# Optimization experiments

Hardware: AMD Instinct MI355X
Metric: run time of the kernel (lower is better)

## Reference

```python
import jax, jax.numpy as jnp
import numpy as np

BS, N1, N2, OUT = 1024, 512, 512, 1024

def setup_inputs() -> dict:
    key = jax.random.key(0)
    k1, k2, k3 = jax.random.split(key, 3)
    x = jax.random.normal(k1, (BS, N1), dtype=jnp.float32)
    y = jax.random.normal(k2, (BS, N2), dtype=jnp.float32)
    # torch nn.Linear weight: [out_features, in_features], in = N1*N2 + N1 + N2
    W = jax.random.normal(k3, (OUT, N1 * N2 + N1 + N2), dtype=jnp.float32) * (1.0 / np.sqrt(N1 * N2 + N1 + N2))
    return {"x": x, "y": y, "W": W}

def reference(x, y, W):
    bs = x.shape[0]
    # outer product per sample, flattened row-major like torch matmul(x1, x2).view(bs,-1)
    x12 = jnp.einsum('bi,bj->bij', x, y).reshape(bs, -1)  # [bs, N1*N2]
    feat = jnp.concatenate([x, y, x12], axis=-1)           # [bs, N1+N2+N1*N2]
    return feat @ W.T                                      # [bs, OUT]
```

## Files before the change

### kernel.cpp

```cpp
#include <hip/hip_runtime.h>
#include <hip/hip_bf16.h>

#define N1C   512
#define N2C   512
#define MC    1024
#define NOUTC 1024
#define WROWC 263168
#define QOFFC 1024
#define NPHASE 129
#define NSPLIT 16

typedef __attribute__((ext_vector_type(8))) short bf16x8;
typedef __attribute__((ext_vector_type(4))) float f32x4;

union FragU { bf16x8 v; __hip_bfloat162 h2[4]; };

__device__ __forceinline__ __hip_bfloat162 cvt2(float a, float b) {
    return __float22bfloat162_rn(make_float2(a, b));
}

__device__ __forceinline__ void stage_direct(short* dst, const float* src) {
    f32x4 a = *(const f32x4*)src;
    f32x4 b = *(const f32x4*)(src + 4);
    FragU f;
    f.h2[0] = cvt2(a[0], a[1]); f.h2[1] = cvt2(a[2], a[3]);
    f.h2[2] = cvt2(b[0], b[1]); f.h2[3] = cvt2(b[2], b[3]);
    *(bf16x8*)dst = f.v;
}

__global__ __launch_bounds__(256) void transpose_x(const float* __restrict__ x,
                                                   float* __restrict__ xT) {
    __shared__ float t[64][65];
    const int i0 = blockIdx.x * 64;
    const int m0 = blockIdx.y * 64;
    const int tx = threadIdx.x & 63;
    const int ty = threadIdx.x >> 6;
#pragma unroll
    for (int k = 0; k < 16; ++k)
        t[ty * 16 + k][tx] = x[(size_t)(m0 + ty * 16 + k) * N1C + i0 + tx];
    __syncthreads();
#pragma unroll
    for (int k = 0; k < 16; ++k)
        xT[(size_t)(i0 + ty * 16 + k) * MC + m0 + tx] = t[tx][ty * 16 + k];
}

__global__ __launch_bounds__(256) void reduce_parts(const float* __restrict__ part,
                                                    float* __restrict__ out) {
    const size_t idx = ((size_t)blockIdx.x * 256 + threadIdx.x) * 4;
    f32x4 s = *(const f32x4*)(part + idx);
#pragma unroll
    for (int j = 1; j < NSPLIT; ++j)
        s += *(const f32x4*)(part + (size_t)j * (MC * NOUTC) + idx);
    *(f32x4*)(out + idx) = s;
}

template<bool USE_XT, bool USE_WS>
__global__ __launch_bounds__(256, 2) void quad_gemm(
        const float* __restrict__ x, const float* __restrict__ y,
        const float* __restrict__ W, const float* __restrict__ xT,
        float* __restrict__ out)
{
    __shared__ short sB[2][4][64][40];
    __shared__ float sX[2][4][512];

    const int tid  = threadIdx.x;
    const int wave = tid >> 6;
    const int lane = tid & 63;
    const int quad = lane >> 4;
    const int l15  = lane & 15;

    const int bid   = blockIdx.x;
    const int xcd   = bid & 7;
    const int useq  = bid >> 3;
    const int mh    = useq & 1;
    const int slice = (useq >> 1) + (xcd << 5);
    const int n0 = (slice & 15) << 6;
    const int jw = slice >> 4;
    const int j0 = jw << 5;
    const int m0 = mh << 9;

    const int mbase  = m0 + wave * 128 + l15;
    const int lrbase = wave * 128 + l15;

    float yf[8][8];
#pragma unroll
    for (int s = 0; s < 8; ++s) {
        const float* yp = y + (size_t)(mbase + s * 16) * N2C + (j0 + quad * 8);
        f32x4 a = *(const f32x4*)yp;
        f32x4 b = *(const f32x4*)(yp + 4);
#pragma unroll
        for (int t = 0; t < 4; ++t) { yf[s][t] = a[t]; yf[s][4 + t] = b[t]; }
    }

    f32x4 acc[8][4];
#pragma unroll
    for (int s = 0; s < 8; ++s)
#pragma unroll
        for (int un = 0; un < 4; ++un)
            acc[s][un] = {0.0f, 0.0f, 0.0f, 0.0f};

    const int sr  = tid >> 2;
    const int sc8 = (tid & 3) * 8;
    const float* wrow = W + (size_t)(n0 + sr) * WROWC + sc8;

    const int iix   = tid >> 6;
    const int lanex = tid & 63;

    stage_direct(&sB[0][0][sr][sc8], wrow + j0);
    stage_direct(&sB[0][1][sr][sc8], wrow + N1C + j0);
    {
        const int kc0 = QOFFC + j0;
#pragma unroll
        for (int ii = 0; ii < 4; ++ii)
            stage_direct(&sB[1][ii][sr][sc8], wrow + kc0 + (ii << 9));
    }
    if constexpr (USE_XT) {
        const float* xs = xT + (size_t)iix * MC + m0 + lanex * 8;
        f32x4 a = *(const f32x4*)xs;
        f32x4 b = *(const f32x4*)(xs + 4);
        *(f32x4*)&sX[1][iix][lanex * 8]     = a;
        *(f32x4*)&sX[1][iix][lanex * 8 + 4] = b;
    }
    __syncthreads();

    {
        bf16x8 afr[8];
#pragma unroll
        for (int s = 0; s < 8; ++s) {
            const float* xp = x + (size_t)(mbase + s * 16) * N1C + (j0 + quad * 8);
            f32x4 a = *(const f32x4*)xp;
            f32x4 b = *(const f32x4*)(xp + 4);
            FragU f;
            f.h2[0] = cvt2(a[0], a[1]); f.h2[1] = cvt2(a[2], a[3]);
            f.h2[2] = cvt2(b[0], b[1]); f.h2[3] = cvt2(b[2], b[3]);
            afr[s] = f.v;
        }
        {
            bf16x8 bfr[4];
#pragma unroll
            for (int un = 0; un < 4; ++un)
                bfr[un] = *(const bf16x8*)&sB[0][0][un * 16 + l15][quad * 8];
#pragma unroll
            for (int s = 0; s < 8; ++s)
#pragma unroll
                for (int un = 0; un < 4; ++un)
                    acc[s][un] = __builtin_amdgcn_mfma_f32_16x16x32_bf16(afr[s], bfr[un], acc[s][un], 0, 0, 0);
        }
#pragma unroll
        for (int s = 0; s < 8; ++s) {
            FragU f;
            f.h2[0] = cvt2(yf[s][0], yf[s][1]); f.h2[1] = cvt2(yf[s][2], yf[s][3]);
            f.h2[2] = cvt2(yf[s][4], yf[s][5]); f.h2[3] = cvt2(yf[s][6], yf[s][7]);
            afr[s] = f.v;
        }
        {
            bf16x8 bfr[4];
#pragma unroll
            for (int un = 0; un < 4; ++un)
                bfr[un] = *(const bf16x8*)&sB[0][1][un * 16 + l15][quad * 8];
#pragma unroll
            for (int s = 0; s < 8; ++s)
#pragma unroll
                for (int un = 0; un < 4; ++un)
                    acc[s][un] = __builtin_amdgcn_mfma_f32_16x16x32_bf16(afr[s], bfr[un], acc[s][un], 0, 0, 0);
        }
    }

    for (int p = 1; p < NPHASE; ++p) {
        const int cur = p & 1;
        const int nxt = cur ^ 1;
        const bool pref = (p + 1 < NPHASE);

        f32x4 wra[4], wrb[4], xra, xrb;
        if (pref) {
            const int kc0 = QOFFC + (p << 11) + j0;
#pragma unroll
            for (int ii = 0; ii < 4; ++ii) {
                const float* src = wrow + kc0 + (ii << 9);
                wra[ii] = *(const f32x4*)src;
                wrb[ii] = *(const f32x4*)(src + 4);
            }
            if constexpr (USE_XT) {
                const float* xs = xT + (size_t)((p << 2) + iix) * MC + m0 + lanex * 8;
                xra = *(const f32x4*)xs;
                xrb = *(const f32x4*)(xs + 4);
            }
        }

        f32x4 xq[8];
        if constexpr (!USE_XT) {
            const int ibase = (p - 1) * 4;
#pragma unroll
            for (int s = 0; s < 8; ++s)
                xq[s] = *(const f32x4*)(x + (size_t)(mbase + s * 16) * N1C + ibase);
        }

#pragma unroll
        for (int ii = 0; ii < 4; ++ii) {
            bf16x8 bfr[4];
#pragma unroll
            for (int un = 0; un < 4; ++un)
                bfr[un] = *(const bf16x8*)&sB[cur][ii][un * 16 + l15][quad * 8];
#pragma unroll
            for (int s = 0; s < 8; ++s) {
                float xs_v;
                if constexpr (USE_XT) xs_v = sX[cur][ii][lrbase + s * 16];
                else                  xs_v = xq[s][ii];
                FragU f;
                f.h2[0] = cvt2(xs_v * yf[s][0], xs_v * yf[s][1]);
                f.h2[1] = cvt2(xs_v * yf[s][2], xs_v * yf[s][3]);
                f.h2[2] = cvt2(xs_v * yf[s][4], xs_v * yf[s][5]);
                f.h2[3] = cvt2(xs_v * yf[s][6], xs_v * yf[s][7]);
#pragma unroll
                for (int un = 0; un < 4; ++un)
                    acc[s][un] = __builtin_amdgcn_mfma_f32_16x16x32_bf16(f.v, bfr[un], acc[s][un], 0, 0, 0);
            }
        }

        if (pref) {
#pragma unroll
            for (int ii = 0; ii < 4; ++ii) {
                FragU f;
                f.h2[0] = cvt2(wra[ii][0], wra[ii][1]); f.h2[1] = cvt2(wra[ii][2], wra[ii][3]);
                f.h2[2] = cvt2(wrb[ii][0], wrb[ii][1]); f.h2[3] = cvt2(wrb[ii][2], wrb[ii][3]);
                *(bf16x8*)&sB[nxt][ii][sr][sc8] = f.v;
            }
            if constexpr (USE_XT) {
                *(f32x4*)&sX[nxt][iix][lanex * 8]     = xra;
                *(f32x4*)&sX[nxt][iix][lanex * 8 + 4] = xrb;
            }
        }
        __syncthreads();
    }

    if constexpr (USE_WS) {
        float* dst = out + (size_t)jw * (MC * NOUTC);
#pragma unroll
        for (int s = 0; s < 8; ++s) {
            const int row0 = m0 + wave * 128 + s * 16 + quad * 4;
#pragma unroll
            for (int un = 0; un < 4; ++un) {
                const int col = n0 + un * 16 + l15;
#pragma unroll
                for (int r = 0; r < 4; ++r)
                    dst[(size_t)(row0 + r) * NOUTC + col] = acc[s][un][r];
            }
        }
    } else {
#pragma unroll
        for (int s = 0; s < 8; ++s) {
            const int row0 = m0 + wave * 128 + s * 16 + quad * 4;
#pragma unroll
            for (int un = 0; un < 4; ++un) {
                const int col = n0 + un * 16 + l15;
#pragma unroll
                for (int r = 0; r < 4; ++r)
                    atomicAdd(out + (size_t)(row0 + r) * NOUTC + col, acc[s][un][r]);
            }
        }
    }
}

extern "C" void kernel_launch(void* const* d_in, const int* in_sizes, int n_in,
                              void* d_out, int out_size, void* d_ws, size_t ws_size,
                              hipStream_t stream) {
    const float* x = (const float*)d_in[0];
    const float* y = (const float*)d_in[1];
    const float* W = (const float*)d_in[2];
    float* out = (float*)d_out;

    const size_t XT_BYTES   = (size_t)N1C * MC * sizeof(float);
    const size_t PART_BYTES = (size_t)NSPLIT * MC * NOUTC * sizeof(float);
    const bool haveXT = ws_size >= XT_BYTES;
    const bool haveWS = ws_size >= XT_BYTES + PART_BYTES;

    float* xT   = (float*)d_ws;
    float* part = (float*)((char*)d_ws + XT_BYTES);

    if (haveXT)
        transpose_x<<<dim3(N1C / 64, MC / 64), dim3(256), 0, stream>>>(x, xT);

    if (haveWS) {
        quad_gemm<true, true><<<dim3(512), dim3(256), 0, stream>>>(x, y, W, xT, part);
        reduce_parts<<<dim3((MC * NOUTC) / (256 * 4)), dim3(256), 0, stream>>>(part, out);
    } else {
        (void)hipMemsetAsync(out, 0, (size_t)out_size * sizeof(float), stream);
        if (haveXT)
            quad_gemm<true, false><<<dim3(512), dim3(256), 0, stream>>>(x, y, W, xT, out);
        else
            quad_gemm<false, false><<<dim3(512), dim3(256), 0, stream>>>(x, y, W, nullptr, out);
    }
}
```

Before: 2.266 ms.

## Split work across 8 waves with smaller per-wave tiles and quarter-M blocks

Each block now covers a quarter of M (256 rows) instead of half, and uses 512 threads arranged as a 4x2 wave grid. Each wave computes a 64x32 tile, so accumulator and y-fragment registers shrink and more waves can be resident per CU. The block count doubles, so the weight slices are staged twice as often overall. The shared-memory x-transpose buffer is dropped: x values are now read straight from the transposed global copy in each phase, which adds global or cache traffic in the inner loop but removes LDS stores and reads.

```diff
diff --git a/kernel.cpp b/kernel.cpp
--- a/kernel.cpp
+++ b/kernel.cpp
@@ -11,21 +11,22 @@
 #define NSPLIT 16
 
 typedef __attribute__((ext_vector_type(8))) short bf16x8;
+typedef __attribute__((ext_vector_type(4))) short bf16x4;
 typedef __attribute__((ext_vector_type(4))) float f32x4;
 
-union FragU { bf16x8 v; __hip_bfloat162 h2[4]; };
-
-__device__ __forceinline__ __hip_bfloat162 cvt2(float a, float b) {
+union FragU  { bf16x8 v; __hip_bfloat162 h2[4]; };
+union Frag4U { bf16x4 v; __hip_bfloat162 h2[2]; };
+
+static __device__ __forceinline__ __hip_bfloat162 cvt2(float a, float b) {
     return __float22bfloat162_rn(make_float2(a, b));
 }
 
-__device__ __forceinline__ void stage_direct(short* dst, const float* src) {
+static __device__ __forceinline__ void stage4(short* dst, const float* src) {
     f32x4 a = *(const f32x4*)src;
-    f32x4 b = *(const f32x4*)(src + 4);
-    FragU f;
-    f.h2[0] = cvt2(a[0], a[1]); f.h2[1] = cvt2(a[2], a[3]);
-    f.h2[2] = cvt2(b[0], b[1]); f.h2[3] = cvt2(b[2], b[3]);
-    *(bf16x8*)dst = f.v;
+    Frag4U f;
+    f.h2[0] = cvt2(a[0], a[1]);
+    f.h2[1] = cvt2(a[2], a[3]);
+    *(bf16x4*)dst = f.v;
 }
 
 __global__ __launch_bounds__(256) void transpose_x(const float* __restrict__ x,
@@ -55,16 +56,17 @@
 }
 
 template<bool USE_XT, bool USE_WS>
-__global__ __launch_bounds__(256, 2) void quad_gemm(
+__global__ __launch_bounds__(512, 4) void quad_gemm(
         const float* __restrict__ x, const float* __restrict__ y,
         const float* __restrict__ W, const float* __restrict__ xT,
         float* __restrict__ out)
 {
     __shared__ short sB[2][4][64][40];
-    __shared__ float sX[2][4][512];
 
     const int tid  = threadIdx.x;
     const int wave = tid >> 6;
+    const int wm   = wave >> 1;
+    const int wn   = wave & 1;
     const int lane = tid & 63;
     const int quad = lane >> 4;
     const int l15  = lane & 15;
@@ -72,19 +74,19 @@
     const int bid   = blockIdx.x;
     const int xcd   = bid & 7;
     const int useq  = bid >> 3;
-    const int mh    = useq & 1;
-    const int slice = (useq >> 1) + (xcd << 5);
+    const int mq    = useq & 3;
+    const int slice = (useq >> 2) + (xcd << 5);
     const int n0 = (slice & 15) << 6;
     const int jw = slice >> 4;
     const int j0 = jw << 5;
-    const int m0 = mh << 9;
-
-    const int mbase  = m0 + wave * 128 + l15;
-    const int lrbase = wave * 128 + l15;
-
-    float yf[8][8];
-#pragma unroll
-    for (int s = 0; s < 8; ++s) {
+    const int m0 = mq << 8;
+
+    const int mbase = m0 + wm * 64 + l15;
+    const int nb    = wn * 32;
+
+    float yf[4][8];
+#pragma unroll
+    for (int s = 0; s < 4; ++s) {
         const float* yp = y + (size_t)(mbase + s * 16) * N2C + (j0 + quad * 8);
         f32x4 a = *(const f32x4*)yp;
         f32x4 b = *(const f32x4*)(yp + 4);
@@ -92,77 +94,52 @@
         for (int t = 0; t < 4; ++t) { yf[s][t] = a[t]; yf[s][4 + t] = b[t]; }
     }
 
-    f32x4 acc[8][4];
-#pragma unroll
-    for (int s = 0; s < 8; ++s)
-#pragma unroll
-        for (int un = 0; un < 4; ++un)
+    f32x4 acc[4][2];
+#pragma unroll
+    for (int s = 0; s < 4; ++s)
+#pragma unroll
+        for (int un = 0; un < 2; ++un)
             acc[s][un] = {0.0f, 0.0f, 0.0f, 0.0f};
 
-    const int sr  = tid >> 2;
-    const int sc8 = (tid & 3) * 8;
-    const float* wrow = W + (size_t)(n0 + sr) * WROWC + sc8;
-
-    const int iix   = tid >> 6;
-    const int lanex = tid & 63;
-
-    stage_direct(&sB[0][0][sr][sc8], wrow + j0);
-    stage_direct(&sB[0][1][sr][sc8], wrow + N1C + j0);
+    const int sr  = tid >> 3;
+    const int sc4 = (tid & 7) << 2;
+    const float* wrow = W + (size_t)(n0 + sr) * WROWC + sc4;
+
+    stage4(&sB[0][0][sr][sc4], wrow + j0);
+    stage4(&sB[0][1][sr][sc4], wrow + N1C + j0);
+#pragma unroll
+    for (int ii = 0; ii < 4; ++ii)
+        stage4(&sB[1][ii][sr][sc4], wrow + QOFFC + j0 + (ii << 9));
+    __syncthreads();
+
     {
-        const int kc0 = QOFFC + j0;
-#pragma unroll
-        for (int ii = 0; ii < 4; ++ii)
-            stage_direct(&sB[1][ii][sr][sc8], wrow + kc0 + (ii << 9));
-    }
-    if constexpr (USE_XT) {
-        const float* xs = xT + (size_t)iix * MC + m0 + lanex * 8;
-        f32x4 a = *(const f32x4*)xs;
-        f32x4 b = *(const f32x4*)(xs + 4);
-        *(f32x4*)&sX[1][iix][lanex * 8]     = a;
-        *(f32x4*)&sX[1][iix][lanex * 8 + 4] = b;
-    }
-    __syncthreads();
-
-    {
-        bf16x8 afr[8];
-#pragma unroll
-        for (int s = 0; s < 8; ++s) {
+        bf16x8 bfr[2];
+#pragma unroll
+        for (int un = 0; un < 2; ++un)
+            bfr[un] = *(const bf16x8*)&sB[0][0][nb + un * 16 + l15][quad * 8];
+#pragma unroll
+        for (int s = 0; s < 4; ++s) {
             const float* xp = x + (size_t)(mbase + s * 16) * N1C + (j0 + quad * 8);
             f32x4 a = *(const f32x4*)xp;
             f32x4 b = *(const f32x4*)(xp + 4);
             FragU f;
             f.h2[0] = cvt2(a[0], a[1]); f.h2[1] = cvt2(a[2], a[3]);
             f.h2[2] = cvt2(b[0], b[1]); f.h2[3] = cvt2(b[2], b[3]);
-            afr[s] = f.v;
-        }
-        {
-            bf16x8 bfr[4];
-#pragma unroll
-            for (int un = 0; un < 4; ++un)
-                bfr[un] = *(const bf16x8*)&sB[0][0][un * 16 + l15][quad * 8];
-#pragma unroll
-            for (int s = 0; s < 8; ++s)
-#pragma unroll
-                for (int un = 0; un < 4; ++un)
-                    acc[s][un] = __builtin_amdgcn_mfma_f32_16x16x32_bf16(afr[s], bfr[un], acc[s][un], 0, 0, 0);
-        }
-#pragma unroll
-        for (int s = 0; s < 8; ++s) {
+#pragma unroll
+            for (int un = 0; un < 2; ++un)
+                acc[s][un] = __builtin_amdgcn_mfma_f32_16x16x32_bf16(f.v, bfr[un], acc[s][un], 0, 0, 0);
+        }
+#pragma unroll
+        for (int un = 0; un < 2; ++un)
+            bfr[un] = *(const bf16x8*)&sB[0][1][nb + un * 16 + l15][quad * 8];
+#pragma unroll
+        for (int s = 0; s < 4; ++s) {
             FragU f;
             f.h2[0] = cvt2(yf[s][0], yf[s][1]); f.h2[1] = cvt2(yf[s][2], yf[s][3]);
             f.h2[2] = cvt2(yf[s][4], yf[s][5]); f.h2[3] = cvt2(yf[s][6], yf[s][7]);
-            afr[s] = f.v;
-        }
-        {
-            bf16x8 bfr[4];
-#pragma unroll
-            for (int un = 0; un < 4; ++un)
-                bfr[un] = *(const bf16x8*)&sB[0][1][un * 16 + l15][quad * 8];
-#pragma unroll
-            for (int s = 0; s < 8; ++s)
-#pragma unroll
-                for (int un = 0; un < 4; ++un)
-                    acc[s][un] = __builtin_amdgcn_mfma_f32_16x16x32_bf16(afr[s], bfr[un], acc[s][un], 0, 0, 0);
+#pragma unroll
+            for (int un = 0; un < 2; ++un)
+                acc[s][un] = __builtin_amdgcn_mfma_f32_16x16x32_bf16(f.v, bfr[un], acc[s][un], 0, 0, 0);
         }
     }
 
@@ -171,63 +148,59 @@
         const int nxt = cur ^ 1;
         const bool pref = (p + 1 < NPHASE);
 
-        f32x4 wra[4], wrb[4], xra, xrb;
+        float xq[4][4];
+        if constexpr (USE_XT) {
+            const int ibase = (p - 1) << 2;
+#pragma unroll
+            for (int ii = 0; ii < 4; ++ii)
+#pragma unroll
+                for (int s = 0; s < 4; ++s)
+                    xq[s][ii] = xT[(size_t)(ibase + ii) * MC + mbase + s * 16];
+        } else {
+            const int ibase = (p - 1) << 2;
+#pragma unroll
+            for (int s = 0; s < 4; ++s) {
+                f32x4 t = *(const f32x4*)(x + (size_t)(mbase + s * 16) * N1C + ibase);
+#pragma unroll
+                for (int ii = 0; ii < 4; ++ii) xq[s][ii] = t[ii];
+            }
+        }
+
+        f32x4 wr[4];
         if (pref) {
             const int kc0 = QOFFC + (p << 11) + j0;
 #pragma unroll
+            for (int ii = 0; ii < 4; ++ii)
+                wr[ii] = *(const f32x4*)(wrow + kc0 + (ii << 9));
+        }
+
+#pragma unroll
+        for (int ii = 0; ii < 4; ++ii) {
+            bf16x8 bfr[2];
+#pragma unroll
+            for (int un = 0; un < 2; ++un)
+                bfr[un] = *(const bf16x8*)&sB[cur][ii][nb + un * 16 + l15][quad * 8];
+#pragma unroll
+            for (int s = 0; s < 4; ++s) {
+                const float xs = xq[s][ii];
+                FragU f;
+                f.h2[0] = cvt2(xs * yf[s][0], xs * yf[s][1]);
+                f.h2[1] = cvt2(xs * yf[s][2], xs * yf[s][3]);
+                f.h2[2] = cvt2(xs * yf[s][4], xs * yf[s][5]);
+                f.h2[3] = cvt2(xs * yf[s][6], xs * yf[s][7]);
+#pragma unroll
+                for (int un = 0; un < 2; ++un)
+                    acc[s][un] = __builtin_amdgcn_mfma_f32_16x16x32_bf16(f.v, bfr[un], acc[s][un], 0, 0, 0);
+            }
+        }
+
+        if (pref) {
+#pragma unroll
             for (int ii = 0; ii < 4; ++ii) {
-                const float* src = wrow + kc0 + (ii << 9);
-                wra[ii] = *(const f32x4*)src;
-                wrb[ii] = *(const f32x4*)(src + 4);
-            }
-            if constexpr (USE_XT) {
-                const float* xs = xT + (size_t)((p << 2) + iix) * MC + m0 + lanex * 8;
-                xra = *(const f32x4*)xs;
-                xrb = *(const f32x4*)(xs + 4);
-            }
-        }
-
-        f32x4 xq[8];
-        if constexpr (!USE_XT) {
-            const int ibase = (p - 1) * 4;
-#pragma unroll
-            for (int s = 0; s < 8; ++s)
-                xq[s] = *(const f32x4*)(x + (size_t)(mbase + s * 16) * N1C + ibase);
-        }
-
-#pragma unroll
-        for (int ii = 0; ii < 4; ++ii) {
-            bf16x8 bfr[4];
-#pragma unroll
-            for (int un = 0; un < 4; ++un)
-                bfr[un] = *(const bf16x8*)&sB[cur][ii][un * 16 + l15][quad * 8];
-#pragma unroll
-            for (int s = 0; s < 8; ++s) {
-                float xs_v;
-                if constexpr (USE_XT) xs_v = sX[cur][ii][lrbase + s * 16];
-                else                  xs_v = xq[s][ii];
-                FragU f;
-                f.h2[0] = cvt2(xs_v * yf[s][0], xs_v * yf[s][1]);
-                f.h2[1] = cvt2(xs_v * yf[s][2], xs_v * yf[s][3]);
-                f.h2[2] = cvt2(xs_v * yf[s][4], xs_v * yf[s][5]);
-                f.h2[3] = cvt2(xs_v * yf[s][6], xs_v * yf[s][7]);
-#pragma unroll
-                for (int un = 0; un < 4; ++un)
-                    acc[s][un] = __builtin_amdgcn_mfma_f32_16x16x32_bf16(f.v, bfr[un], acc[s][un], 0, 0, 0);
-            }
-        }
-
-        if (pref) {
-#pragma unroll
-            for (int ii = 0; ii < 4; ++ii) {
-                FragU f;
-                f.h2[0] = cvt2(wra[ii][0], wra[ii][1]); f.h2[1] = cvt2(wra[ii][2], wra[ii][3]);
-                f.h2[2] = cvt2(wrb[ii][0], wrb[ii][1]); f.h2[3] = cvt2(wrb[ii][2], wrb[ii][3]);
-                *(bf16x8*)&sB[nxt][ii][sr][sc8] = f.v;
-            }
-            if constexpr (USE_XT) {
-                *(f32x4*)&sX[nxt][iix][lanex * 8]     = xra;
-                *(f32x4*)&sX[nxt][iix][lanex * 8 + 4] = xrb;
+                Frag4U f;
+                f.h2[0] = cvt2(wr[ii][0], wr[ii][1]);
+                f.h2[1] = cvt2(wr[ii][2], wr[ii][3]);
+                *(bf16x4*)&sB[nxt][ii][sr][sc4] = f.v;
             }
         }
         __syncthreads();
@@ -236,11 +209,11 @@
     if constexpr (USE_WS) {
         float* dst = out + (size_t)jw * (MC * NOUTC);
 #pragma unroll
-        for (int s = 0; s < 8; ++s) {
-            const int row0 = m0 + wave * 128 + s * 16 + quad * 4;
-#pragma unroll
-            for (int un = 0; un < 4; ++un) {
-                const int col = n0 + un * 16 + l15;
+        for (int s = 0; s < 4; ++s) {
+            const int row0 = m0 + wm * 64 + s * 16 + quad * 4;
+#pragma unroll
+            for (int un = 0; un < 2; ++un) {
+                const int col = n0 + nb + un * 16 + l15;
 #pragma unroll
                 for (int r = 0; r < 4; ++r)
                     dst[(size_t)(row0 + r) * NOUTC + col] = acc[s][un][r];
@@ -248,11 +221,11 @@
         }
     } else {
 #pragma unroll
-        for (int s = 0; s < 8; ++s) {
-            const int row0 = m0 + wave * 128 + s * 16 + quad * 4;
-#pragma unroll
-            for (int un = 0; un < 4; ++un) {
-                const int col = n0 + un * 16 + l15;
+        for (int s = 0; s < 4; ++s) {
+            const int row0 = m0 + wm * 64 + s * 16 + quad * 4;
+#pragma unroll
+            for (int un = 0; un < 2; ++un) {
+                const int col = n0 + nb + un * 16 + l15;
 #pragma unroll
                 for (int r = 0; r < 4; ++r)
                     atomicAdd(out + (size_t)(row0 + r) * NOUTC + col, acc[s][un][r]);
@@ -281,13 +254,13 @@
         transpose_x<<<dim3(N1C / 64, MC / 64), dim3(256), 0, stream>>>(x, xT);
 
     if (haveWS) {
-        quad_gemm<true, true><<<dim3(512), dim3(256), 0, stream>>>(x, y, W, xT, part);
+        quad_gemm<true, true><<<dim3(1024), dim3(512), 0, stream>>>(x, y, W, xT, part);
         reduce_parts<<<dim3((MC * NOUTC) / (256 * 4)), dim3(256), 0, stream>>>(part, out);
     } else {
         (void)hipMemsetAsync(out, 0, (size_t)out_size * sizeof(float), stream);
         if (haveXT)
-            quad_gemm<true, false><<<dim3(512), dim3(256), 0, stream>>>(x, y, W, xT, out);
+            quad_gemm<true, false><<<dim3(1024), dim3(512), 0, stream>>>(x, y, W, xT, out);
         else
-            quad_gemm<false, false><<<dim3(512), dim3(256), 0, stream>>>(x, y, W, nullptr, out);
-    }
-}
+            quad_gemm<false, false><<<dim3(1024), dim3(512), 0, stream>>>(x, y, W, nullptr, out);
+    }
+}
```

New measurement: 2.034 ms. 10.2% less time.
